# Optimization experiments

Measured on AMD Instinct MI355X. Metric: run time of the kernel, lower is better.

## Reference

```python
import jax, jax.numpy as jnp
import numpy as np

N_CLASSES = 19
N_BINS = 10
EPS = 1e-13


def setup_inputs() -> dict:
    key = jax.random.key(0)
    k1, k2 = jax.random.split(key)
    output = jax.random.normal(k1, (1, N_CLASSES, 1024, 2048), dtype=jnp.float32)
    target = jax.random.randint(k2, (1, 1024, 2048), 0, N_CLASSES, dtype=jnp.int32)
    return {"output": output, "target": target}


def reference(output, target):
    # output: [B, C, H, W] logits; target: [B, H, W] int labels
    B, C, H, W = output.shape
    p = jax.nn.softmax(output, axis=1)  # [B, C, H, W]

    # Bin i covers (i/N_BINS, (i+1)/N_BINS]; p == 0 belongs to no bin.
    bin_idx = jnp.clip(jnp.ceil(p * N_BINS).astype(jnp.int32) - 1, 0, N_BINS - 1)
    valid = p > 0

    cls = jnp.arange(C, dtype=jnp.int32)[None, :, None, None]  # idealMap per class
    # Combined (class, bin) segment id; invalid pixels dumped into extra segment.
    seg = jnp.where(valid, cls * N_BINS + bin_idx, C * N_BINS).reshape(-1)
    n_seg = C * N_BINS + 1

    p_flat = p.reshape(-1)
    conf_sum = jax.ops.segment_sum(p_flat, seg, num_segments=n_seg)[:-1].reshape(C, N_BINS)
    no_pred = jax.ops.segment_sum(jnp.ones_like(p_flat), seg, num_segments=n_seg)[:-1].reshape(C, N_BINS)
    correct = (target[:, None, :, :] == cls).astype(p.dtype)  # idealMap == target
    no_acc = jax.ops.segment_sum(correct.reshape(-1), seg, num_segments=n_seg)[:-1].reshape(C, N_BINS)

    avg_acc = no_acc / (no_pred + EPS)
    avg_conf = conf_sum / (no_pred + EPS)
    loss = jnp.sum((avg_acc - avg_conf) ** 2 * (no_pred / jnp.sum(no_pred)))
    return loss
```

## Files before the change

kernel.cpp:

```cpp
#include <hip/hip_runtime.h>

#define NC 19
#define NB 10
#define NCELL (NC * NB)
#define NPART (3 * NCELL + 2 * NC)
#define REP 4

__global__ __launch_bounds__(256, 3) void cce_pass1(
    const float* __restrict__ logits, const int* __restrict__ tgt,
    float* __restrict__ gacc, int hw)
{
    constexpr int O_CONF = 0;
    constexpr int O_PRED = REP * NCELL;
    constexpr int O_ACC  = 2 * REP * NCELL;
    constexpr int O_PSUM = 3 * REP * NCELL;
    constexpr int O_INV  = 3 * REP * NCELL + REP * NC;
    constexpr int LDS_N  = O_INV + NC;

    __shared__ float lds[LDS_N];
    for (int i = threadIdx.x; i < LDS_N; i += blockDim.x) lds[i] = 0.0f;
    __syncthreads();

    const int rep = threadIdx.x & (REP - 1);
    float psum[NC];
#pragma unroll
    for (int c = 0; c < NC; ++c) psum[c] = 0.0f;

    const int ngroups  = hw >> 2;
    const int tid      = blockIdx.x * blockDim.x + threadIdx.x;
    const int nthreads = gridDim.x * blockDim.x;

    for (int g = tid; g < ngroups; g += nthreads) {
        float x[NC][4];
#pragma unroll
        for (int c = 0; c < NC; ++c) {
            float4 v = *reinterpret_cast<const float4*>(logits + (size_t)c * hw + 4 * (size_t)g);
            x[c][0] = v.x; x[c][1] = v.y; x[c][2] = v.z; x[c][3] = v.w;
        }
        const int4 t4 = *reinterpret_cast<const int4*>(tgt + 4 * (size_t)g);
        const int tt[4] = {t4.x, t4.y, t4.z, t4.w};

#pragma unroll
        for (int k = 0; k < 4; ++k) {
            float m = x[0][k];
#pragma unroll
            for (int c = 1; c < NC; ++c) m = fmaxf(m, x[c][k]);
            float e[NC];
            float s = 0.0f;
#pragma unroll
            for (int c = 0; c < NC; ++c) { e[c] = expf(x[c][k] - m); s += e[c]; }
            const float rinv = 1.0f / s;
            const int t = tt[k];
            float ptgt = 0.0f;
#pragma unroll
            for (int c = 0; c < NC; ++c) {
                const float p = e[c] * rinv;
                psum[c] += p;
                if (c == t) ptgt = p;
                const float pb = p * 10.0f;
                if (pb > 1.0f) {
                    int bin = (int)ceilf(pb) - 1;
                    if (bin > NB - 1) bin = NB - 1;
                    atomicAdd(&lds[O_CONF + rep * NCELL + c * NB + bin], p);
                    atomicAdd(&lds[O_PRED + rep * NCELL + c * NB + bin], 1.0f);
                }
                if (!(p > 0.0f)) atomicAdd(&lds[O_INV + c], 1.0f);
            }
            if (ptgt > 0.0f) {
                int bt = (int)ceilf(ptgt * 10.0f) - 1;
                if (bt < 0) bt = 0;
                if (bt > NB - 1) bt = NB - 1;
                atomicAdd(&lds[O_ACC + rep * NCELL + t * NB + bt], 1.0f);
            }
        }
    }
#pragma unroll
    for (int c = 0; c < NC; ++c)
        atomicAdd(&lds[O_PSUM + rep * NC + c], psum[c]);
    __syncthreads();

    for (int j = threadIdx.x; j < NPART; j += blockDim.x) {
        float v = 0.0f;
        if (j < NCELL) {
            for (int r = 0; r < REP; ++r) v += lds[O_CONF + r * NCELL + j];
        } else if (j < 2 * NCELL) {
            for (int r = 0; r < REP; ++r) v += lds[O_PRED + r * NCELL + (j - NCELL)];
        } else if (j < 3 * NCELL) {
            for (int r = 0; r < REP; ++r) v += lds[O_ACC + r * NCELL + (j - 2 * NCELL)];
        } else if (j < 3 * NCELL + NC) {
            for (int r = 0; r < REP; ++r) v += lds[O_PSUM + r * NC + (j - 3 * NCELL)];
        } else {
            v = lds[O_INV + (j - 3 * NCELL - NC)];
        }
        atomicAdd(&gacc[j], v);
    }
}

__global__ void cce_pass2(const float* __restrict__ gacc, float* __restrict__ out, int hw)
{
    __shared__ double fin[NPART];
    const int j = threadIdx.x;
    if (j < NPART) fin[j] = (double)gacc[j];
    __syncthreads();

    if (j < NC) {
        double spred = 0.0, sconf = 0.0;
        for (int b = 1; b < NB; ++b) {
            spred += fin[NCELL + j * NB + b];
            sconf += fin[j * NB + b];
        }
        const double validc = (double)hw - fin[3 * NCELL + NC + j];
        fin[NCELL + j * NB] = validc - spred;
        fin[j * NB]         = fin[3 * NCELL + j] - sconf;
    }
    __syncthreads();

    if (j < 64) {
        double tot = 0.0;
        for (int c = j; c < NCELL; c += 64) tot += fin[NCELL + c];
#pragma unroll
        for (int o = 32; o > 0; o >>= 1) tot += __shfl_down(tot, o);
        tot = __shfl(tot, 0);

        double loss = 0.0;
        for (int c = j; c < NCELL; c += 64) {
            const double pred = fin[NCELL + c];
            const double conf = fin[c];
            const double acc  = fin[2 * NCELL + c];
            const double d    = (acc - conf) / (pred + 1e-13);
            loss += d * d * (pred / tot);
        }
#pragma unroll
        for (int o = 32; o > 0; o >>= 1) loss += __shfl_down(loss, o);
        if (j == 0) out[0] = (float)loss;
    }
}

extern "C" void kernel_launch(void* const* d_in, const int* in_sizes, int n_in,
                              void* d_out, int out_size, void* d_ws, size_t ws_size,
                              hipStream_t stream)
{
    const float* logits = (const float*)d_in[0];
    const int*   tgt    = (const int*)d_in[1];
    float*       gacc   = (float*)d_ws;
    const int    hw     = in_sizes[1];

    hipMemsetAsync(gacc, 0, NPART * sizeof(float), stream);
    cce_pass1<<<512, 256, 0, stream>>>(logits, tgt, gacc, hw);
    cce_pass2<<<1, 640, 0, stream>>>(gacc, (float*)d_out, hw);
}
```

Before: 271.8 us.

## Process two pixels per thread, use fast exp/rcp, more blocks, slotted global atomics

Each thread now handles two pixels per iteration with float2 loads instead of four with float4, which cuts register pressure. The launch grows to 2048 blocks with no occupancy hint. Softmax uses __expf and the hardware reciprocal instead of precise expf and division. The per-class invalid check runs only when the minimum probability is non-positive. Global partial sums are spread over 16 slots, which pass2 then reduces, to lower contention on global atomics. The fast math changes precision slightly, and the extra blocks add more LDS init and flush overhead.

New measurement: 296.2 us. 1.09x slower.

```diff
diff --git a/kernel.cpp b/kernel.cpp
--- a/kernel.cpp
+++ b/kernel.cpp
@@ -5,8 +5,11 @@
 #define NCELL (NC * NB)
 #define NPART (3 * NCELL + 2 * NC)
 #define REP 4
+#define NSLOT 16
+#define BLOCKS 2048
+#define TPB 256
 
-__global__ __launch_bounds__(256, 3) void cce_pass1(
+__global__ __launch_bounds__(TPB) void cce_pass1(
     const float* __restrict__ logits, const int* __restrict__ tgt,
     float* __restrict__ gacc, int hw)
 {
@@ -18,7 +21,7 @@
     constexpr int LDS_N  = O_INV + NC;
 
     __shared__ float lds[LDS_N];
-    for (int i = threadIdx.x; i < LDS_N; i += blockDim.x) lds[i] = 0.0f;
+    for (int i = threadIdx.x; i < LDS_N; i += TPB) lds[i] = 0.0f;
     __syncthreads();
 
     const int rep = threadIdx.x & (REP - 1);
@@ -26,52 +29,74 @@
 #pragma unroll
     for (int c = 0; c < NC; ++c) psum[c] = 0.0f;
 
-    const int ngroups  = hw >> 2;
-    const int tid      = blockIdx.x * blockDim.x + threadIdx.x;
-    const int nthreads = gridDim.x * blockDim.x;
+    const int ngroups  = hw >> 1;
+    const int tid      = blockIdx.x * TPB + threadIdx.x;
+    const int nthreads = gridDim.x * TPB;
 
     for (int g = tid; g < ngroups; g += nthreads) {
-        float x[NC][4];
+        float xa[NC], xb[NC];
 #pragma unroll
         for (int c = 0; c < NC; ++c) {
-            float4 v = *reinterpret_cast<const float4*>(logits + (size_t)c * hw + 4 * (size_t)g);
-            x[c][0] = v.x; x[c][1] = v.y; x[c][2] = v.z; x[c][3] = v.w;
+            const float2 v = *reinterpret_cast<const float2*>(
+                logits + (size_t)c * hw + 2 * (size_t)g);
+            xa[c] = v.x; xb[c] = v.y;
         }
-        const int4 t4 = *reinterpret_cast<const int4*>(tgt + 4 * (size_t)g);
-        const int tt[4] = {t4.x, t4.y, t4.z, t4.w};
+        const int2 t2 = *reinterpret_cast<const int2*>(tgt + 2 * (size_t)g);
 
+        float m0 = xa[0], m1 = xb[0];
 #pragma unroll
-        for (int k = 0; k < 4; ++k) {
-            float m = x[0][k];
+        for (int c = 1; c < NC; ++c) { m0 = fmaxf(m0, xa[c]); m1 = fmaxf(m1, xb[c]); }
+
+        float s0 = 0.0f, s1 = 0.0f;
 #pragma unroll
-            for (int c = 1; c < NC; ++c) m = fmaxf(m, x[c][k]);
-            float e[NC];
-            float s = 0.0f;
+        for (int c = 0; c < NC; ++c) {
+            xa[c] = __expf(xa[c] - m0); s0 += xa[c];
+            xb[c] = __expf(xb[c] - m1); s1 += xb[c];
+        }
+        const float r0 = __builtin_amdgcn_rcpf(s0);
+        const float r1 = __builtin_amdgcn_rcpf(s1);
+
+        float pt0 = 0.0f, pt1 = 0.0f, pmin0 = 1.0f, pmin1 = 1.0f;
 #pragma unroll
-            for (int c = 0; c < NC; ++c) { e[c] = expf(x[c][k] - m); s += e[c]; }
-            const float rinv = 1.0f / s;
-            const int t = tt[k];
-            float ptgt = 0.0f;
+        for (int c = 0; c < NC; ++c) {
+            const float p0 = xa[c] * r0;
+            const float p1 = xb[c] * r1;
+            psum[c] += p0 + p1;
+            if (c == t2.x) pt0 = p0;
+            if (c == t2.y) pt1 = p1;
+            pmin0 = fminf(pmin0, p0);
+            pmin1 = fminf(pmin1, p1);
+            const float q0 = p0 * 10.0f, q1 = p1 * 10.0f;
+            if (q0 > 1.0f) {
+                int b = (int)ceilf(q0) - 1; b = b > NB - 1 ? NB - 1 : b;
+                atomicAdd(&lds[O_CONF + rep * NCELL + c * NB + b], p0);
+                atomicAdd(&lds[O_PRED + rep * NCELL + c * NB + b], 1.0f);
+            }
+            if (q1 > 1.0f) {
+                int b = (int)ceilf(q1) - 1; b = b > NB - 1 ? NB - 1 : b;
+                atomicAdd(&lds[O_CONF + rep * NCELL + c * NB + b], p1);
+                atomicAdd(&lds[O_PRED + rep * NCELL + c * NB + b], 1.0f);
+            }
+        }
+        if (pt0 > 0.0f) {
+            int b = (int)ceilf(pt0 * 10.0f) - 1;
+            b = b < 0 ? 0 : (b > NB - 1 ? NB - 1 : b);
+            atomicAdd(&lds[O_ACC + rep * NCELL + t2.x * NB + b], 1.0f);
+        }
+        if (pt1 > 0.0f) {
+            int b = (int)ceilf(pt1 * 10.0f) - 1;
+            b = b < 0 ? 0 : (b > NB - 1 ? NB - 1 : b);
+            atomicAdd(&lds[O_ACC + rep * NCELL + t2.y * NB + b], 1.0f);
+        }
+        if (!(pmin0 > 0.0f)) {
 #pragma unroll
-            for (int c = 0; c < NC; ++c) {
-                const float p = e[c] * rinv;
-                psum[c] += p;
-                if (c == t) ptgt = p;
-                const float pb = p * 10.0f;
-                if (pb > 1.0f) {
-                    int bin = (int)ceilf(pb) - 1;
-                    if (bin > NB - 1) bin = NB - 1;
-                    atomicAdd(&lds[O_CONF + rep * NCELL + c * NB + bin], p);
-                    atomicAdd(&lds[O_PRED + rep * NCELL + c * NB + bin], 1.0f);
-                }
-                if (!(p > 0.0f)) atomicAdd(&lds[O_INV + c], 1.0f);
-            }
-            if (ptgt > 0.0f) {
-                int bt = (int)ceilf(ptgt * 10.0f) - 1;
-                if (bt < 0) bt = 0;
-                if (bt > NB - 1) bt = NB - 1;
-                atomicAdd(&lds[O_ACC + rep * NCELL + t * NB + bt], 1.0f);
-            }
+            for (int c = 0; c < NC; ++c)
+                if (!(xa[c] * r0 > 0.0f)) atomicAdd(&lds[O_INV + c], 1.0f);
+        }
+        if (!(pmin1 > 0.0f)) {
+#pragma unroll
+            for (int c = 0; c < NC; ++c)
+                if (!(xb[c] * r1 > 0.0f)) atomicAdd(&lds[O_INV + c], 1.0f);
         }
     }
 #pragma unroll
@@ -79,7 +104,8 @@
         atomicAdd(&lds[O_PSUM + rep * NC + c], psum[c]);
     __syncthreads();
 
-    for (int j = threadIdx.x; j < NPART; j += blockDim.x) {
+    float* slot = gacc + (size_t)(blockIdx.x & (NSLOT - 1)) * NPART;
+    for (int j = threadIdx.x; j < NPART; j += TPB) {
         float v = 0.0f;
         if (j < NCELL) {
             for (int r = 0; r < REP; ++r) v += lds[O_CONF + r * NCELL + j];
@@ -92,7 +118,7 @@
         } else {
             v = lds[O_INV + (j - 3 * NCELL - NC)];
         }
-        atomicAdd(&gacc[j], v);
+        atomicAdd(&slot[j], v);
     }
 }
 
@@ -100,7 +126,11 @@
 {
     __shared__ double fin[NPART];
     const int j = threadIdx.x;
-    if (j < NPART) fin[j] = (double)gacc[j];
+    if (j < NPART) {
+        double v = 0.0;
+        for (int s = 0; s < NSLOT; ++s) v += (double)gacc[(size_t)s * NPART + j];
+        fin[j] = v;
+    }
     __syncthreads();
 
     if (j < NC) {
@@ -145,7 +175,7 @@
     float*       gacc   = (float*)d_ws;
     const int    hw     = in_sizes[1];
 
-    hipMemsetAsync(gacc, 0, NPART * sizeof(float), stream);
-    cce_pass1<<<512, 256, 0, stream>>>(logits, tgt, gacc, hw);
+    hipMemsetAsync(gacc, 0, (size_t)NSLOT * NPART * sizeof(float), stream);
+    cce_pass1<<<BLOCKS, TPB, 0, stream>>>(logits, tgt, gacc, hw);
     cce_pass2<<<1, 640, 0, stream>>>(gacc, (float*)d_out, hw);
 }
```
